# Performance work log

Hardware: AMD Instinct MI355X
Metric: run time of the kernel (lower is better)

Reference implementation:

```python
import jax, jax.numpy as jnp
import numpy as np

B = 131072
MV_IN, PC_IN, D, OUT = 256, 128, 128, 128
LN_EPS = 1e-5
NORM_EPS = 1e-9


def _lin_init(key, fan_in, fan_out):
    kw, kb = jax.random.split(key)
    s = 1.0 / np.sqrt(fan_in)
    W = jax.random.uniform(kw, (fan_in, fan_out), minval=-s, maxval=s, dtype=jnp.float32)
    b = jax.random.uniform(kb, (fan_out,), minval=-s, maxval=s, dtype=jnp.float32)
    return W, b


def setup_inputs() -> dict:
    key = jax.random.key(0)
    ks = jax.random.split(key, 12)
    mv_enc = jax.random.normal(ks[0], (B, MV_IN), dtype=jnp.float32)
    pc_enc = jax.random.normal(ks[1], (B, PC_IN), dtype=jnp.float32)
    Wq_mv, bq_mv = _lin_init(ks[2], MV_IN, D)
    Wk_mv, bk_mv = _lin_init(ks[3], MV_IN, D)
    Wv_mv, bv_mv = _lin_init(ks[4], MV_IN, D)
    Wq_pc, bq_pc = _lin_init(ks[5], PC_IN, D)
    Wk_pc, bk_pc = _lin_init(ks[6], PC_IN, D)
    Wv_pc, bv_pc = _lin_init(ks[7], PC_IN, D)
    Wq_c, bq_c = _lin_init(ks[8], D, D)
    Wk_c, bk_c = _lin_init(ks[9], D, D)
    Wv_c, bv_c = _lin_init(ks[10], D, D)
    Wp, bp = _lin_init(ks[11], D, OUT)
    ln_g = jnp.ones((OUT,), dtype=jnp.float32)
    ln_b = jnp.zeros((OUT,), dtype=jnp.float32)
    return dict(mv_enc=mv_enc, pc_enc=pc_enc,
                Wq_mv=Wq_mv, bq_mv=bq_mv, Wk_mv=Wk_mv, bk_mv=bk_mv, Wv_mv=Wv_mv, bv_mv=bv_mv,
                Wq_pc=Wq_pc, bq_pc=bq_pc, Wk_pc=Wk_pc, bk_pc=bk_pc, Wv_pc=Wv_pc, bv_pc=bv_pc,
                Wq_c=Wq_c, bq_c=bq_c, Wk_c=Wk_c, bk_c=bk_c, Wv_c=Wv_c, bv_c=bv_c,
                Wp=Wp, bp=bp, ln_g=ln_g, ln_b=ln_b)


def _sa(q, k, v):
    # scaled-dot-product self-attention with residual (+v), seq len = 2
    d = q.shape[-1]
    scores = jnp.einsum('bqd,bkd->bqk', q, k) / jnp.sqrt(jnp.asarray(d, q.dtype))
    a = jax.nn.softmax(scores, axis=-1)
    return jnp.einsum('bqk,bkd->bqd', a, v) + v


def _rep2(t):
    # torch .repeat(1, 2, 1) on a [B,1,D] tensor
    return jnp.concatenate([t, t], axis=1)


def reference(mv_enc, pc_enc,
              Wq_mv, bq_mv, Wk_mv, bk_mv, Wv_mv, bv_mv,
              Wq_pc, bq_pc, Wk_pc, bk_pc, Wv_pc, bv_pc,
              Wq_c, bq_c, Wk_c, bk_c, Wv_c, bv_c,
              Wp, bp, ln_g, ln_b):
    mv = mv_enc[:, None, :]  # [B,1,256]
    pc = pc_enc[:, None, :]  # [B,1,128]
    q_mv = mv @ Wq_mv + bq_mv
    k_mv = mv @ Wk_mv + bk_mv
    v_mv = mv @ Wv_mv + bv_mv
    q_pc = pc @ Wq_pc + bq_pc
    k_pc = pc @ Wk_pc + bk_pc
    v_pc = pc @ Wv_pc + bv_pc
    v_cat = jnp.concatenate([v_mv, v_pc], axis=1)  # [B,2,128]
    res_mv = _sa(_rep2(q_mv), _rep2(k_mv), v_cat).max(axis=1, keepdims=True)  # [B,1,128]
    res_pc = _sa(_rep2(q_pc), _rep2(k_pc), v_cat).max(axis=1, keepdims=True)  # [B,1,128]
    x = jnp.concatenate([res_mv, res_pc], axis=1)  # [B,2,128]
    q_c = x @ Wq_c + bq_c
    k_c = x @ Wk_c + bk_c
    v_c = x @ Wv_c + bv_c
    res = _sa(q_c, k_c, v_c).max(axis=1)  # [B,128]
    h = res @ Wp + bp
    mu = h.mean(axis=-1, keepdims=True)
    var = ((h - mu) ** 2).mean(axis=-1, keepdims=True)
    h = (h - mu) * jax.lax.rsqrt(var + LN_EPS) * ln_g + ln_b
    h = jax.nn.selu(h)
    return h / (jnp.linalg.norm(h, axis=1, keepdims=True) + NORM_EPS)
```

## Files before the change

kernel.cpp:

```cpp
#include <hip/hip_runtime.h>
#include <math.h>


typedef float f32x4 __attribute__((ext_vector_type(4)));
typedef short s16x8 __attribute__((ext_vector_type(8)));

__device__ __forceinline__ unsigned short f2bf(float x) {
    unsigned u = __builtin_bit_cast(unsigned, x);
    unsigned r = u + 0x7fffu + ((u >> 16) & 1u);
    return (unsigned short)(r >> 16);
}
__device__ __forceinline__ float bf2f(unsigned short h) {
    return __builtin_bit_cast(float, ((unsigned)h) << 16);
}

__global__ void prep_w2(const float* __restrict__ Wv_c, const float* __restrict__ Wp,
                        const float* __restrict__ bv_c, const float* __restrict__ bp,
                        float* __restrict__ W2, float* __restrict__ b2) {
    int j = threadIdx.x;
    int i = blockIdx.x;
    if (i < 128) {
        float s = 0.f;
        for (int k = 0; k < 128; ++k) s = fmaf(Wv_c[i * 128 + k], Wp[k * 128 + j], s);
        W2[i * 128 + j] = s;
    } else {
        float s = 0.f;
        for (int k = 0; k < 128; ++k) s = fmaf(bv_c[k], Wp[k * 128 + j], s);
        b2[j] = 2.f * s + bp[j];
    }
}

__global__ void pack_frags(const float* __restrict__ W, unsigned short* __restrict__ out) {
    int f = blockIdx.x;
    int l = threadIdx.x;
    int c = f >> 3, t = f & 7;
    int col = t * 16 + (l & 15);
    int k0 = c * 32 + (l >> 4) * 8;
    unsigned short hi[8], lo[8];
    #pragma unroll
    for (int i = 0; i < 8; ++i) {
        float x = W[(k0 + i) * 128 + col];
        unsigned short h = f2bf(x);
        hi[i] = h;
        lo[i] = f2bf(x - bf2f(h));
    }
    unsigned short* base = out + (size_t)f * 1024 + (size_t)l * 8;
    #pragma unroll
    for (int i = 0; i < 8; ++i) base[i] = hi[i];
    #pragma unroll
    for (int i = 0; i < 8; ++i) base[512 + i] = lo[i];
}

__launch_bounds__(256, 2)
__global__ void fused_main(const float* __restrict__ mv, const float* __restrict__ pc,
                           const unsigned short* __restrict__ Fmv,
                           const unsigned short* __restrict__ Fpc,
                           const unsigned short* __restrict__ Fw2,
                           const float* __restrict__ b_mv, const float* __restrict__ b_pc,
                           const float* __restrict__ b2v,
                           const float* __restrict__ ln_g, const float* __restrict__ ln_b,
                           float* __restrict__ out) {
    __shared__ unsigned int r2lds[4][32][128];
    const int tid = threadIdx.x;
    const int wv  = tid >> 6;
    const int l   = tid & 63;
    const int lg  = l >> 4;
    const int ll  = l & 15;
    const int rowbase = blockIdx.x * 128 + wv * 32;

    const f32x4 vz = {0.f, 0.f, 0.f, 0.f};
    f32x4 acc1[2][8], acc2[2][8];
    #pragma unroll
    for (int s = 0; s < 2; ++s)
        #pragma unroll
        for (int t = 0; t < 8; ++t) { acc1[s][t] = vz; acc2[s][t] = vz; }

    #pragma unroll 1
    for (int c = 0; c < 8; ++c) {
        s16x8 ah[2], al[2];
        #pragma unroll
        for (int s = 0; s < 2; ++s) {
            const float* ap = mv + (size_t)(rowbase + s * 16 + ll) * 256 + c * 32 + lg * 8;
            f32x4 x0 = *(const f32x4*)ap;
            f32x4 x1 = *(const f32x4*)(ap + 4);
            #pragma unroll
            for (int i = 0; i < 4; ++i) {
                unsigned short h0 = f2bf(x0[i]);
                ah[s][i] = (short)h0;
                al[s][i] = (short)f2bf(x0[i] - bf2f(h0));
                unsigned short h1 = f2bf(x1[i]);
                ah[s][4 + i] = (short)h1;
                al[s][4 + i] = (short)f2bf(x1[i] - bf2f(h1));
            }
        }
        const unsigned short* fb = Fmv + (size_t)c * 8192 + (size_t)l * 8;
        #pragma unroll
        for (int t = 0; t < 8; ++t) {
            s16x8 bh = *(const s16x8*)(fb + t * 1024);
            s16x8 bl = *(const s16x8*)(fb + t * 1024 + 512);
            #pragma unroll
            for (int s = 0; s < 2; ++s) {
                acc1[s][t] = __builtin_amdgcn_mfma_f32_16x16x32_bf16(ah[s], bh, acc1[s][t], 0, 0, 0);
                acc1[s][t] = __builtin_amdgcn_mfma_f32_16x16x32_bf16(al[s], bh, acc1[s][t], 0, 0, 0);
                acc1[s][t] = __builtin_amdgcn_mfma_f32_16x16x32_bf16(ah[s], bl, acc1[s][t], 0, 0, 0);
            }
        }
    }

    #pragma unroll 1
    for (int c = 0; c < 4; ++c) {
        s16x8 ah[2], al[2];
        #pragma unroll
        for (int s = 0; s < 2; ++s) {
            const float* ap = pc + (size_t)(rowbase + s * 16 + ll) * 128 + c * 32 + lg * 8;
            f32x4 x0 = *(const f32x4*)ap;
            f32x4 x1 = *(const f32x4*)(ap + 4);
            #pragma unroll
            for (int i = 0; i < 4; ++i) {
                unsigned short h0 = f2bf(x0[i]);
                ah[s][i] = (short)h0;
                al[s][i] = (short)f2bf(x0[i] - bf2f(h0));
                unsigned short h1 = f2bf(x1[i]);
                ah[s][4 + i] = (short)h1;
                al[s][4 + i] = (short)f2bf(x1[i] - bf2f(h1));
            }
        }
        const unsigned short* fb = Fpc + (size_t)c * 8192 + (size_t)l * 8;
        #pragma unroll
        for (int t = 0; t < 8; ++t) {
            s16x8 bh = *(const s16x8*)(fb + t * 1024);
            s16x8 bl = *(const s16x8*)(fb + t * 1024 + 512);
            #pragma unroll
            for (int s = 0; s < 2; ++s) {
                acc2[s][t] = __builtin_amdgcn_mfma_f32_16x16x32_bf16(ah[s], bh, acc2[s][t], 0, 0, 0);
                acc2[s][t] = __builtin_amdgcn_mfma_f32_16x16x32_bf16(al[s], bh, acc2[s][t], 0, 0, 0);
                acc2[s][t] = __builtin_amdgcn_mfma_f32_16x16x32_bf16(ah[s], bl, acc2[s][t], 0, 0, 0);
            }
        }
    }

    #pragma unroll
    for (int t = 0; t < 8; ++t) {
        float bm  = b_mv[t * 16 + ll];
        float bpc = b_pc[t * 16 + ll];
        #pragma unroll
        for (int s = 0; s < 2; ++s) {
            #pragma unroll
            for (int j = 0; j < 4; ++j) {
                float x1 = acc1[s][t][j] + bm;
                float x2 = acc2[s][t][j] + bpc;
                float r2 = (x1 + x2) + 2.f * fmaxf(x1, x2);
                unsigned short h  = f2bf(r2);
                unsigned short lo = f2bf(r2 - bf2f(h));
                r2lds[wv][s * 16 + lg * 4 + j][t * 16 + ll] = ((unsigned)lo << 16) | (unsigned)h;
            }
        }
    }
    __syncthreads();

    f32x4 acch[2][8];
    #pragma unroll
    for (int s = 0; s < 2; ++s)
        #pragma unroll
        for (int t = 0; t < 8; ++t) acch[s][t] = vz;

    #pragma unroll 1
    for (int c = 0; c < 4; ++c) {
        s16x8 ah[2], al[2];
        #pragma unroll
        for (int s = 0; s < 2; ++s) {
            const unsigned int* rp = &r2lds[wv][s * 16 + ll][c * 32 + lg * 8];
            #pragma unroll
            for (int i = 0; i < 8; ++i) {
                unsigned u = rp[i];
                ah[s][i] = (short)(u & 0xffffu);
                al[s][i] = (short)(u >> 16);
            }
        }
        const unsigned short* fb = Fw2 + (size_t)c * 8192 + (size_t)l * 8;
        #pragma unroll
        for (int t = 0; t < 8; ++t) {
            s16x8 bh = *(const s16x8*)(fb + t * 1024);
            s16x8 bl = *(const s16x8*)(fb + t * 1024 + 512);
            #pragma unroll
            for (int s = 0; s < 2; ++s) {
                acch[s][t] = __builtin_amdgcn_mfma_f32_16x16x32_bf16(ah[s], bh, acch[s][t], 0, 0, 0);
                acch[s][t] = __builtin_amdgcn_mfma_f32_16x16x32_bf16(al[s], bh, acch[s][t], 0, 0, 0);
                acch[s][t] = __builtin_amdgcn_mfma_f32_16x16x32_bf16(ah[s], bl, acch[s][t], 0, 0, 0);
            }
        }
    }

    float b2c[8], bg[8], bb[8];
    #pragma unroll
    for (int t = 0; t < 8; ++t) {
        b2c[t] = b2v[t * 16 + ll];
        bg[t]  = ln_g[t * 16 + ll];
        bb[t]  = ln_b[t * 16 + ll];
    }
    #pragma unroll
    for (int s = 0; s < 2; ++s) {
        #pragma unroll
        for (int j = 0; j < 4; ++j) {
            float v[8];
            float sum = 0.f, ssq = 0.f;
            #pragma unroll
            for (int t = 0; t < 8; ++t) {
                float h = acch[s][t][j] + b2c[t];
                v[t] = h;
                sum += h;
                ssq = fmaf(h, h, ssq);
            }
            #pragma unroll
            for (int o = 1; o < 16; o <<= 1) {
                sum += __shfl_xor(sum, o);
                ssq += __shfl_xor(ssq, o);
            }
            float mu  = sum * 0.0078125f;
            float var = ssq * 0.0078125f - mu * mu;
            float rs  = 1.f / sqrtf(var + 1e-5f);
            float s2  = 0.f;
            #pragma unroll
            for (int t = 0; t < 8; ++t) {
                float hn = (v[t] - mu) * rs * bg[t] + bb[t];
                float m  = hn > 0.f ? hn : 1.6732632423543772f * expm1f(hn);
                m = 1.0507009873554805f * m;
                v[t] = m;
                s2 = fmaf(m, m, s2);
            }
            #pragma unroll
            for (int o = 1; o < 16; o <<= 1) s2 += __shfl_xor(s2, o);
            float sc = 1.f / (sqrtf(s2) + 1e-9f);
            int row = rowbase + s * 16 + lg * 4 + j;
            float* op = out + (size_t)row * 128 + ll;
            #pragma unroll
            for (int t = 0; t < 8; ++t) op[t * 16] = v[t] * sc;
        }
    }
}

extern "C" void kernel_launch(void* const* d_in, const int* in_sizes, int n_in,
                              void* d_out, int out_size, void* d_ws, size_t ws_size,
                              hipStream_t stream) {
    const float* mv    = (const float*)d_in[0];
    const float* pc    = (const float*)d_in[1];
    const float* Wv_mv = (const float*)d_in[6];
    const float* bv_mv = (const float*)d_in[7];
    const float* Wv_pc = (const float*)d_in[12];
    const float* bv_pc = (const float*)d_in[13];
    const float* Wv_c  = (const float*)d_in[18];
    const float* bv_c  = (const float*)d_in[19];
    const float* Wp    = (const float*)d_in[20];
    const float* bp    = (const float*)d_in[21];
    const float* ln_g  = (const float*)d_in[22];
    const float* ln_b  = (const float*)d_in[23];
    float* out = (float*)d_out;

    char* ws = (char*)d_ws;
    float* W2 = (float*)ws;
    float* b2 = (float*)(ws + 65536);
    unsigned short* Fmv = (unsigned short*)(ws + 66048);
    unsigned short* Fpc = Fmv + 65536;
    unsigned short* Fw2 = Fpc + 32768;

    prep_w2<<<129, 128, 0, stream>>>(Wv_c, Wp, bv_c, bp, W2, b2);
    pack_frags<<<64, 64, 0, stream>>>(Wv_mv, Fmv);
    pack_frags<<<32, 64, 0, stream>>>(Wv_pc, Fpc);
    pack_frags<<<32, 64, 0, stream>>>(W2, Fw2);

    fused_main<<<1024, 256, 0, stream>>>(mv, pc, Fmv, Fpc, Fw2,
                                         bv_mv, bv_pc, b2, ln_g, ln_b, out);
}
```

Baseline: 356.4 us.

## Fuse prep kernels, swap MFMA operand order, pass intermediates via shuffles instead of LDS

The four weight-preparation kernels become one launch that also computes the folded Wv_c·Wp product directly into packed fragments. In the main kernel the first two GEMMs swap operand roles so the accumulator layout comes out transposed. The intermediate then moves between lanes through cross-lane shuffles instead of an LDS round trip plus __syncthreads. Dropping the 64KB of shared memory and raising launch bounds to 3 blocks per CU is meant to improve occupancy, at the risk of register pressure and extra shuffle instructions.

```diff
diff --git a/kernel.cpp b/kernel.cpp
--- a/kernel.cpp
+++ b/kernel.cpp
@@ -1,57 +1,77 @@
 #include <hip/hip_runtime.h>
+#include <hip/hip_bf16.h>
 #include <math.h>
 
 
 typedef float f32x4 __attribute__((ext_vector_type(4)));
 typedef short s16x8 __attribute__((ext_vector_type(8)));
 
+#define MFMA __builtin_amdgcn_mfma_f32_16x16x32_bf16
+
 __device__ __forceinline__ unsigned short f2bf(float x) {
-    unsigned u = __builtin_bit_cast(unsigned, x);
-    unsigned r = u + 0x7fffu + ((u >> 16) & 1u);
-    return (unsigned short)(r >> 16);
-}
-__device__ __forceinline__ float bf2f(unsigned short h) {
-    return __builtin_bit_cast(float, ((unsigned)h) << 16);
-}
-
-__global__ void prep_w2(const float* __restrict__ Wv_c, const float* __restrict__ Wp,
-                        const float* __restrict__ bv_c, const float* __restrict__ bp,
-                        float* __restrict__ W2, float* __restrict__ b2) {
-    int j = threadIdx.x;
-    int i = blockIdx.x;
-    if (i < 128) {
-        float s = 0.f;
-        for (int k = 0; k < 128; ++k) s = fmaf(Wv_c[i * 128 + k], Wp[k * 128 + j], s);
-        W2[i * 128 + j] = s;
+    __hip_bfloat16 h = __float2bfloat16(x);
+    return __builtin_bit_cast(unsigned short, h);
+}
+__device__ __forceinline__ float bf2f(unsigned short u) {
+    return __builtin_bit_cast(float, ((unsigned)u) << 16);
+}
+__device__ __forceinline__ unsigned packsplit(float x) {
+    unsigned short h = f2bf(x);
+    unsigned short l = f2bf(x - bf2f(h));
+    return ((unsigned)l << 16) | (unsigned)h;
+}
+
+__global__ void prep_all(const float* __restrict__ Wv_mv, const float* __restrict__ Wv_pc,
+                         const float* __restrict__ Wv_c,  const float* __restrict__ Wp,
+                         const float* __restrict__ bv_c,  const float* __restrict__ bp,
+                         unsigned short* __restrict__ Fmv, unsigned short* __restrict__ Fpc,
+                         unsigned short* __restrict__ Fw2, float* __restrict__ b2) {
+    int b = blockIdx.x;
+    int l = threadIdx.x;
+    if (b < 128) {
+        const float* W = nullptr;
+        unsigned short* out = nullptr;
+        int f;
+        bool direct = true;
+        if (b < 64)       { W = Wv_mv; out = Fmv; f = b; }
+        else if (b < 96)  { W = Wv_pc; out = Fpc; f = b - 64; }
+        else              { out = Fw2; f = b - 96; direct = false; }
+        int c = f >> 3, t = f & 7;
+        int col = t * 16 + (l & 15);
+        int k0 = c * 32 + (l >> 4) * 8;
+        unsigned short hi[8], lo[8];
+        #pragma unroll
+        for (int i = 0; i < 8; ++i) {
+            float x;
+            if (direct) {
+                x = W[(size_t)(k0 + i) * 128 + col];
+            } else {
+                float s = 0.f;
+                for (int k = 0; k < 128; ++k)
+                    s = fmaf(Wv_c[(size_t)(k0 + i) * 128 + k], Wp[(size_t)k * 128 + col], s);
+                x = s;
+            }
+            unsigned short h = f2bf(x);
+            hi[i] = h;
+            lo[i] = f2bf(x - bf2f(h));
+        }
+        unsigned short* base = out + (size_t)f * 1024 + (size_t)l * 8;
+        #pragma unroll
+        for (int i = 0; i < 8; ++i) base[i] = hi[i];
+        #pragma unroll
+        for (int i = 0; i < 8; ++i) base[512 + i] = lo[i];
     } else {
-        float s = 0.f;
-        for (int k = 0; k < 128; ++k) s = fmaf(bv_c[k], Wp[k * 128 + j], s);
-        b2[j] = 2.f * s + bp[j];
-    }
-}
-
-__global__ void pack_frags(const float* __restrict__ W, unsigned short* __restrict__ out) {
-    int f = blockIdx.x;
-    int l = threadIdx.x;
-    int c = f >> 3, t = f & 7;
-    int col = t * 16 + (l & 15);
-    int k0 = c * 32 + (l >> 4) * 8;
-    unsigned short hi[8], lo[8];
-    #pragma unroll
-    for (int i = 0; i < 8; ++i) {
-        float x = W[(k0 + i) * 128 + col];
-        unsigned short h = f2bf(x);
-        hi[i] = h;
-        lo[i] = f2bf(x - bf2f(h));
-    }
-    unsigned short* base = out + (size_t)f * 1024 + (size_t)l * 8;
-    #pragma unroll
-    for (int i = 0; i < 8; ++i) base[i] = hi[i];
-    #pragma unroll
-    for (int i = 0; i < 8; ++i) base[512 + i] = lo[i];
-}
-
-__launch_bounds__(256, 2)
+        #pragma unroll
+        for (int rep = 0; rep < 2; ++rep) {
+            int j = l + rep * 64;
+            float s = 0.f;
+            for (int k = 0; k < 128; ++k) s = fmaf(bv_c[k], Wp[(size_t)k * 128 + j], s);
+            b2[j] = 2.f * s + bp[j];
+        }
+    }
+}
+
+__launch_bounds__(256, 3)
 __global__ void fused_main(const float* __restrict__ mv, const float* __restrict__ pc,
                            const unsigned short* __restrict__ Fmv,
                            const unsigned short* __restrict__ Fpc,
@@ -60,7 +80,6 @@
                            const float* __restrict__ b2v,
                            const float* __restrict__ ln_g, const float* __restrict__ ln_b,
                            float* __restrict__ out) {
-    __shared__ unsigned int r2lds[4][32][128];
     const int tid = threadIdx.x;
     const int wv  = tid >> 6;
     const int l   = tid & 63;
@@ -69,124 +88,134 @@
     const int rowbase = blockIdx.x * 128 + wv * 32;
 
     const f32x4 vz = {0.f, 0.f, 0.f, 0.f};
-    f32x4 acc1[2][8], acc2[2][8];
-    #pragma unroll
-    for (int s = 0; s < 2; ++s)
-        #pragma unroll
-        for (int t = 0; t < 8; ++t) { acc1[s][t] = vz; acc2[s][t] = vz; }
+
+    f32x4 acc1[8][2];
+    #pragma unroll
+    for (int tf = 0; tf < 8; ++tf) { acc1[tf][0] = vz; acc1[tf][1] = vz; }
 
     #pragma unroll 1
     for (int c = 0; c < 8; ++c) {
-        s16x8 ah[2], al[2];
-        #pragma unroll
-        for (int s = 0; s < 2; ++s) {
-            const float* ap = mv + (size_t)(rowbase + s * 16 + ll) * 256 + c * 32 + lg * 8;
+        s16x8 dh[2], dl[2];
+        #pragma unroll
+        for (int ts = 0; ts < 2; ++ts) {
+            const float* ap = mv + (size_t)(rowbase + ts * 16 + ll) * 256 + c * 32 + lg * 8;
             f32x4 x0 = *(const f32x4*)ap;
             f32x4 x1 = *(const f32x4*)(ap + 4);
             #pragma unroll
             for (int i = 0; i < 4; ++i) {
-                unsigned short h0 = f2bf(x0[i]);
-                ah[s][i] = (short)h0;
-                al[s][i] = (short)f2bf(x0[i] - bf2f(h0));
-                unsigned short h1 = f2bf(x1[i]);
-                ah[s][4 + i] = (short)h1;
-                al[s][4 + i] = (short)f2bf(x1[i] - bf2f(h1));
+                unsigned p0 = packsplit(x0[i]);
+                dh[ts][i]     = (short)(p0 & 0xffffu);
+                dl[ts][i]     = (short)(p0 >> 16);
+                unsigned p1 = packsplit(x1[i]);
+                dh[ts][4 + i] = (short)(p1 & 0xffffu);
+                dl[ts][4 + i] = (short)(p1 >> 16);
             }
         }
         const unsigned short* fb = Fmv + (size_t)c * 8192 + (size_t)l * 8;
+        #pragma unroll
+        for (int tf = 0; tf < 8; ++tf) {
+            s16x8 wh = *(const s16x8*)(fb + tf * 1024);
+            s16x8 wl = *(const s16x8*)(fb + tf * 1024 + 512);
+            #pragma unroll
+            for (int ts = 0; ts < 2; ++ts) {
+                acc1[tf][ts] = MFMA(wh, dh[ts], acc1[tf][ts], 0, 0, 0);
+                acc1[tf][ts] = MFMA(wl, dh[ts], acc1[tf][ts], 0, 0, 0);
+                acc1[tf][ts] = MFMA(wh, dl[ts], acc1[tf][ts], 0, 0, 0);
+            }
+        }
+    }
+
+    f32x4 acc2[8][2];
+    #pragma unroll
+    for (int tf = 0; tf < 8; ++tf) { acc2[tf][0] = vz; acc2[tf][1] = vz; }
+
+    #pragma unroll 1
+    for (int c = 0; c < 4; ++c) {
+        s16x8 dh[2], dl[2];
+        #pragma unroll
+        for (int ts = 0; ts < 2; ++ts) {
+            const float* ap = pc + (size_t)(rowbase + ts * 16 + ll) * 128 + c * 32 + lg * 8;
+            f32x4 x0 = *(const f32x4*)ap;
+            f32x4 x1 = *(const f32x4*)(ap + 4);
+            #pragma unroll
+            for (int i = 0; i < 4; ++i) {
+                unsigned p0 = packsplit(x0[i]);
+                dh[ts][i]     = (short)(p0 & 0xffffu);
+                dl[ts][i]     = (short)(p0 >> 16);
+                unsigned p1 = packsplit(x1[i]);
+                dh[ts][4 + i] = (short)(p1 & 0xffffu);
+                dl[ts][4 + i] = (short)(p1 >> 16);
+            }
+        }
+        const unsigned short* fb = Fpc + (size_t)c * 8192 + (size_t)l * 8;
+        #pragma unroll
+        for (int tf = 0; tf < 8; ++tf) {
+            s16x8 wh = *(const s16x8*)(fb + tf * 1024);
+            s16x8 wl = *(const s16x8*)(fb + tf * 1024 + 512);
+            #pragma unroll
+            for (int ts = 0; ts < 2; ++ts) {
+                acc2[tf][ts] = MFMA(wh, dh[ts], acc2[tf][ts], 0, 0, 0);
+                acc2[tf][ts] = MFMA(wl, dh[ts], acc2[tf][ts], 0, 0, 0);
+                acc2[tf][ts] = MFMA(wh, dl[ts], acc2[tf][ts], 0, 0, 0);
+            }
+        }
+    }
+
+    unsigned r2p[8][2][4];
+    #pragma unroll
+    for (int tf = 0; tf < 8; ++tf) {
+        #pragma unroll
+        for (int j = 0; j < 4; ++j) {
+            float bm = b_mv[tf * 16 + lg * 4 + j];
+            float bq = b_pc[tf * 16 + lg * 4 + j];
+            #pragma unroll
+            for (int ts = 0; ts < 2; ++ts) {
+                float x1 = acc1[tf][ts][j] + bm;
+                float x2 = acc2[tf][ts][j] + bq;
+                float r2 = (x1 + x2) + 2.f * fmaxf(x1, x2);
+                r2p[tf][ts][j] = packsplit(r2);
+            }
+        }
+    }
+
+    f32x4 acch[2][8];
+    #pragma unroll
+    for (int ts = 0; ts < 2; ++ts)
+        #pragma unroll
+        for (int t = 0; t < 8; ++t) acch[ts][t] = vz;
+
+    const int g0 = (((lg * 2)     ) & 3) * 16 + ll;
+    const int g1 = (((lg * 2) + 1 ) & 3) * 16 + ll;
+    const bool uhi = (lg & 2) != 0;
+
+    #pragma unroll
+    for (int c = 0; c < 4; ++c) {
+        s16x8 ah[2], al[2];
+        #pragma unroll
+        for (int ts = 0; ts < 2; ++ts) {
+            #pragma unroll
+            for (int q = 0; q < 2; ++q) {
+                const int src = q ? g1 : g0;
+                #pragma unroll
+                for (int j = 0; j < 4; ++j) {
+                    unsigned va = __shfl(r2p[2 * c][ts][j], src);
+                    unsigned vb = __shfl(r2p[2 * c + 1][ts][j], src);
+                    unsigned v  = uhi ? vb : va;
+                    ah[ts][q * 4 + j] = (short)(v & 0xffffu);
+                    al[ts][q * 4 + j] = (short)(v >> 16);
+                }
+            }
+        }
+        const unsigned short* fb = Fw2 + (size_t)c * 8192 + (size_t)l * 8;
         #pragma unroll
         for (int t = 0; t < 8; ++t) {
             s16x8 bh = *(const s16x8*)(fb + t * 1024);
             s16x8 bl = *(const s16x8*)(fb + t * 1024 + 512);
             #pragma unroll
-            for (int s = 0; s < 2; ++s) {
-                acc1[s][t] = __builtin_amdgcn_mfma_f32_16x16x32_bf16(ah[s], bh, acc1[s][t], 0, 0, 0);
-                acc1[s][t] = __builtin_amdgcn_mfma_f32_16x16x32_bf16(al[s], bh, acc1[s][t], 0, 0, 0);
-                acc1[s][t] = __builtin_amdgcn_mfma_f32_16x16x32_bf16(ah[s], bl, acc1[s][t], 0, 0, 0);
-            }
-        }
-    }
-
-    #pragma unroll 1
-    for (int c = 0; c < 4; ++c) {
-        s16x8 ah[2], al[2];
-        #pragma unroll
-        for (int s = 0; s < 2; ++s) {
-            const float* ap = pc + (size_t)(rowbase + s * 16 + ll) * 128 + c * 32 + lg * 8;
-            f32x4 x0 = *(const f32x4*)ap;
-            f32x4 x1 = *(const f32x4*)(ap + 4);
-            #pragma unroll
-            for (int i = 0; i < 4; ++i) {
-                unsigned short h0 = f2bf(x0[i]);
-                ah[s][i] = (short)h0;
-                al[s][i] = (short)f2bf(x0[i] - bf2f(h0));
-                unsigned short h1 = f2bf(x1[i]);
-                ah[s][4 + i] = (short)h1;
-                al[s][4 + i] = (short)f2bf(x1[i] - bf2f(h1));
-            }
-        }
-        const unsigned short* fb = Fpc + (size_t)c * 8192 + (size_t)l * 8;
-        #pragma unroll
-        for (int t = 0; t < 8; ++t) {
-            s16x8 bh = *(const s16x8*)(fb + t * 1024);
-            s16x8 bl = *(const s16x8*)(fb + t * 1024 + 512);
-            #pragma unroll
-            for (int s = 0; s < 2; ++s) {
-                acc2[s][t] = __builtin_amdgcn_mfma_f32_16x16x32_bf16(ah[s], bh, acc2[s][t], 0, 0, 0);
-                acc2[s][t] = __builtin_amdgcn_mfma_f32_16x16x32_bf16(al[s], bh, acc2[s][t], 0, 0, 0);
-                acc2[s][t] = __builtin_amdgcn_mfma_f32_16x16x32_bf16(ah[s], bl, acc2[s][t], 0, 0, 0);
-            }
-        }
-    }
-
-    #pragma unroll
-    for (int t = 0; t < 8; ++t) {
-        float bm  = b_mv[t * 16 + ll];
-        float bpc = b_pc[t * 16 + ll];
-        #pragma unroll
-        for (int s = 0; s < 2; ++s) {
-            #pragma unroll
-            for (int j = 0; j < 4; ++j) {
-                float x1 = acc1[s][t][j] + bm;
-                float x2 = acc2[s][t][j] + bpc;
-                float r2 = (x1 + x2) + 2.f * fmaxf(x1, x2);
-                unsigned short h  = f2bf(r2);
-                unsigned short lo = f2bf(r2 - bf2f(h));
-                r2lds[wv][s * 16 + lg * 4 + j][t * 16 + ll] = ((unsigned)lo << 16) | (unsigned)h;
-            }
-        }
-    }
-    __syncthreads();
-
-    f32x4 acch[2][8];
-    #pragma unroll
-    for (int s = 0; s < 2; ++s)
-        #pragma unroll
-        for (int t = 0; t < 8; ++t) acch[s][t] = vz;
-
-    #pragma unroll 1
-    for (int c = 0; c < 4; ++c) {
-        s16x8 ah[2], al[2];
-        #pragma unroll
-        for (int s = 0; s < 2; ++s) {
-            const unsigned int* rp = &r2lds[wv][s * 16 + ll][c * 32 + lg * 8];
-            #pragma unroll
-            for (int i = 0; i < 8; ++i) {
-                unsigned u = rp[i];
-                ah[s][i] = (short)(u & 0xffffu);
-                al[s][i] = (short)(u >> 16);
-            }
-        }
-        const unsigned short* fb = Fw2 + (size_t)c * 8192 + (size_t)l * 8;
-        #pragma unroll
-        for (int t = 0; t < 8; ++t) {
-            s16x8 bh = *(const s16x8*)(fb + t * 1024);
-            s16x8 bl = *(const s16x8*)(fb + t * 1024 + 512);
-            #pragma unroll
-            for (int s = 0; s < 2; ++s) {
-                acch[s][t] = __builtin_amdgcn_mfma_f32_16x16x32_bf16(ah[s], bh, acch[s][t], 0, 0, 0);
-                acch[s][t] = __builtin_amdgcn_mfma_f32_16x16x32_bf16(al[s], bh, acch[s][t], 0, 0, 0);
-                acch[s][t] = __builtin_amdgcn_mfma_f32_16x16x32_bf16(ah[s], bl, acch[s][t], 0, 0, 0);
+            for (int ts = 0; ts < 2; ++ts) {
+                acch[ts][t] = MFMA(ah[ts], bh, acch[ts][t], 0, 0, 0);
+                acch[ts][t] = MFMA(al[ts], bh, acch[ts][t], 0, 0, 0);
+                acch[ts][t] = MFMA(ah[ts], bl, acch[ts][t], 0, 0, 0);
             }
         }
     }
@@ -199,14 +228,14 @@
         bb[t]  = ln_b[t * 16 + ll];
     }
     #pragma unroll
-    for (int s = 0; s < 2; ++s) {
+    for (int ts = 0; ts < 2; ++ts) {
         #pragma unroll
         for (int j = 0; j < 4; ++j) {
             float v[8];
             float sum = 0.f, ssq = 0.f;
             #pragma unroll
             for (int t = 0; t < 8; ++t) {
-                float h = acch[s][t][j] + b2c[t];
+                float h = acch[ts][t][j] + b2c[t];
                 v[t] = h;
                 sum += h;
                 ssq = fmaf(h, h, ssq);
@@ -231,7 +260,7 @@
             #pragma unroll
             for (int o = 1; o < 16; o <<= 1) s2 += __shfl_xor(s2, o);
             float sc = 1.f / (sqrtf(s2) + 1e-9f);
-            int row = rowbase + s * 16 + lg * 4 + j;
+            int row = rowbase + ts * 16 + lg * 4 + j;
             float* op = out + (size_t)row * 128 + ll;
             #pragma unroll
             for (int t = 0; t < 8; ++t) op[t * 16] = v[t] * sc;
@@ -257,17 +286,13 @@
     float* out = (float*)d_out;
 
     char* ws = (char*)d_ws;
-    float* W2 = (float*)ws;
-    float* b2 = (float*)(ws + 65536);
-    unsigned short* Fmv = (unsigned short*)(ws + 66048);
+    unsigned short* Fmv = (unsigned short*)ws;
     unsigned short* Fpc = Fmv + 65536;
     unsigned short* Fw2 = Fpc + 32768;
-
-    prep_w2<<<129, 128, 0, stream>>>(Wv_c, Wp, bv_c, bp, W2, b2);
-    pack_frags<<<64, 64, 0, stream>>>(Wv_mv, Fmv);
-    pack_frags<<<32, 64, 0, stream>>>(Wv_pc, Fpc);
-    pack_frags<<<32, 64, 0, stream>>>(W2, Fw2);
-
+    float* b2 = (float*)(ws + 262144);
+
+    prep_all<<<129, 64, 0, stream>>>(Wv_mv, Wv_pc, Wv_c, Wp, bv_c, bp,
+                                     Fmv, Fpc, Fw2, b2);
     fused_main<<<1024, 256, 0, stream>>>(mv, pc, Fmv, Fpc, Fw2,
                                          bv_mv, bv_pc, b2, ln_g, ln_b, out);
 }
```

Result: slower. 403.1 us (+13.1%).
